# Kernel tuning notes

Measured on AMD Instinct MI355X. Metric: run time of the kernel, lower is better.

Reference implementation:

```python
import jax, jax.numpy as jnp
import numpy as np

N = 50000
E = 400000
C_IN = 32
H = 64
RATIO = 0.5
SEQ_LEN = 5


def setup_inputs() -> dict:
    key = jax.random.key(0)
    ks = jax.random.split(key, 12)
    x = jax.random.normal(ks[0], (N, C_IN), jnp.float32)
    row = jax.random.randint(ks[1], (E,), 0, N, jnp.int32)
    off = jax.random.randint(ks[2], (E,), 1, N, jnp.int32)
    col = ((row + off) % N).astype(jnp.int32)  # no self-loops
    edge_index = jnp.stack([row, col])
    mask = jax.random.uniform(ks[3], (N,)) < 0.5

    def g(k, shape, fan):
        return jax.random.normal(k, shape, jnp.float32) / np.float32(np.sqrt(fan))

    return {
        "x": x, "edge_index": edge_index, "mask": mask,
        "conv0_w": g(ks[4], (C_IN, H), C_IN), "conv0_b": jnp.zeros((H,), jnp.float32),
        "conv1_w": g(ks[5], (H, H), H), "conv1_b": jnp.zeros((H,), jnp.float32),
        "pool_w": g(ks[6], (H,), H),
        "up_w": g(ks[7], (H, H), H), "up_b": jnp.zeros((H,), jnp.float32),
        "lstm0_w_ih": g(ks[8], (4 * H, H), H), "lstm0_w_hh": g(ks[9], (4 * H, H), H),
        "lstm0_b_ih": jnp.zeros((4 * H,), jnp.float32), "lstm0_b_hh": jnp.zeros((4 * H,), jnp.float32),
        "fin_w_ih": g(ks[10], (4 * H, H), H), "fin_w_hh": g(ks[11], (4 * H, H), H),
        "fin_b_ih": jnp.zeros((4 * H,), jnp.float32), "fin_b_hh": jnp.zeros((4 * H,), jnp.float32),
    }


def _coalesce(row, col, w, n):
    # sum duplicate (row, col) entries; output sorted by (row, col)
    key = row.astype(np.int64) * n + col.astype(np.int64)
    uk, inv = np.unique(key, return_inverse=True)
    w2 = np.bincount(inv, weights=w.astype(np.float64), minlength=uk.shape[0]).astype(np.float32)
    return uk // n, uk % n, w2


def _augment_adj(row, col, w, n):
    # remove self loops, add self loops (weight 1), compute A @ A (sparse), remove self loops
    m = row != col
    row = np.concatenate([row[m].astype(np.int64), np.arange(n, dtype=np.int64)])
    col = np.concatenate([col[m].astype(np.int64), np.arange(n, dtype=np.int64)])
    w = np.concatenate([w[m].astype(np.float32), np.ones(n, np.float32)])
    row, col, w = _coalesce(row, col, w, n)  # CSR-ordered
    cnt = np.bincount(row, minlength=n)
    indptr = np.concatenate([[0], np.cumsum(cnt)])
    dk = cnt[col]                      # out-degree of middle node k for each edge (i,k)
    starts = indptr[col]
    total = int(dk.sum())
    seg = np.repeat(np.cumsum(dk) - dk, dk)
    gi = np.repeat(starts, dk) + (np.arange(total) - seg)
    oi = np.repeat(row, dk)
    oj = col[gi]
    ow = np.repeat(w, dk) * w[gi]
    r2, c2, w2 = _coalesce(oi, oj, ow, n)
    m2 = r2 != c2
    return r2[m2], c2[m2], w2[m2]


def _gcn(x, row, col, ew, n, W, b):
    # GCNConv(improved=True): self-loop weight 2.0, symmetric deg^-1/2 normalization,
    # aggregate messages at target (col)
    h = x @ W
    loop = jnp.arange(n, dtype=row.dtype)
    r = jnp.concatenate([row, loop])
    c = jnp.concatenate([col, loop])
    w = jnp.concatenate([ew, jnp.full((n,), 2.0, ew.dtype)])
    deg = jax.ops.segment_sum(w, c, num_segments=n)
    dinv = jnp.where(deg > 0, jax.lax.rsqrt(deg), 0.0)
    norm = dinv[r] * w * dinv[c]
    out = jax.ops.segment_sum(norm[:, None] * h[r], c, num_segments=n)
    return out + b


def _sequences(x, mi):
    # sliding window [idx-L+1, idx] per masked node, zero left-padded
    t = mi[:, None] + jnp.arange(SEQ_LEN)[None, :] - (SEQ_LEN - 1)  # [M, L]
    return jnp.where((t >= 0)[:, :, None], x[jnp.clip(t, 0)], 0.0)


def _lstm_last(seq, w_ih, w_hh, b_ih, b_hh):
    # torch LSTM gate order: i, f, g, o; zero init state; return last hidden
    h = jnp.zeros((seq.shape[0], w_hh.shape[1]), seq.dtype)
    c = jnp.zeros_like(h)
    def step(carry, xt):
        h, c = carry
        g = xt @ w_ih.T + h @ w_hh.T + b_ih + b_hh
        i, f, gg, o = jnp.split(g, 4, axis=-1)
        c = jax.nn.sigmoid(f) * c + jax.nn.sigmoid(i) * jnp.tanh(gg)
        h = jax.nn.sigmoid(o) * jnp.tanh(c)
        return (h, c), None
    (h, _), _ = jax.lax.scan(step, (h, c), jnp.swapaxes(seq, 0, 1))
    return h


def reference(x, edge_index, mask, conv0_w, conv0_b, conv1_w, conv1_b, pool_w,
              up_w, up_b, lstm0_w_ih, lstm0_w_hh, lstm0_b_ih, lstm0_b_hh,
              fin_w_ih, fin_w_hh, fin_b_ih, fin_b_hh):
    n = x.shape[0]
    row0, col0 = edge_index[0], edge_index[1]
    ew0 = jnp.ones((row0.shape[0],), x.dtype)

    # down conv 0
    x1 = jax.nn.relu(_gcn(x, row0, col0, ew0, n, conv0_w, conv0_b))

    # augment_adj: sparse (A+I)^2 without diagonal (structural, constant)
    r2, c2, w2 = _augment_adj(np.asarray(row0), np.asarray(col0),
                              np.ones(row0.shape[0], np.float32), n)

    # TopKPooling: score = tanh((x.w)/||w||), keep top ceil(ratio*n)
    score = jnp.tanh((x1 @ pool_w) / jnp.linalg.norm(pool_w))
    k = int(np.ceil(RATIO * n))
    perm = np.argsort(-np.asarray(score), kind="stable")[:k]
    remap = np.full(n, -1, np.int64)
    remap[perm] = np.arange(k)
    keep = (remap[r2] >= 0) & (remap[c2] >= 0)
    pr = jnp.asarray(remap[r2[keep]].astype(np.int32))
    pc = jnp.asarray(remap[c2[keep]].astype(np.int32))
    pw = jnp.asarray(w2[keep])
    permj = jnp.asarray(perm.astype(np.int32))
    xp = x1[permj] * score[permj][:, None]

    # down conv 1 on pooled graph
    x2 = jax.nn.relu(_gcn(xp, pr, pc, pw, k, conv1_w, conv1_b))

    # up path (depth=1): LSTM over skip features at masked nodes
    mi = jnp.asarray(np.where(np.asarray(mask))[0].astype(np.int32))
    h0 = _lstm_last(_sequences(x1, mi), lstm0_w_ih, lstm0_w_hh, lstm0_b_ih, lstm0_b_hh)
    res = x1.at[mi].set(h0)
    up = jnp.zeros_like(x1).at[permj].set(x2)
    xo = _gcn(res + up, row0, col0, ew0, n, up_w, up_b)  # last level: no activation

    # final LSTM on masked nodes
    hf = _lstm_last(_sequences(xo, mi), fin_w_ih, fin_w_hh, fin_b_ih, fin_b_hh)
    return xo.at[mi].set(hf)
```

## Files before the change

### kernel.cpp

```cpp
#include <hip/hip_runtime.h>
#include <math.h>

#define NN 50000
#define EE 400000
#define CINV 32
#define KKEEP 25000
#define SEQL 5
#define HASH_BITS 20
#define HASH_SIZE (1u<<HASH_BITS)
#define HASH_MASK (HASH_SIZE-1u)
#define HEMPTY 0xFFFFFFFFu
#define PSB 196

typedef float vf4 __attribute__((ext_vector_type(4)));

__device__ __forceinline__ float sigm(float x){ return __builtin_amdgcn_rcpf(1.f+__expf(-x)); }
__device__ __forceinline__ float ftanh(float x){ return 1.f - 2.f*__builtin_amdgcn_rcpf(1.f+__expf(2.f*x)); }

__global__ void k_init(uint2* __restrict__ hash, unsigned* __restrict__ hist,
                       int* __restrict__ degcnt, int* __restrict__ diagint,
                       int* __restrict__ fillc, int* __restrict__ minv,
                       unsigned* scal, unsigned long long* selp,
                       const float* __restrict__ w0, const float* __restrict__ b0i,
                       const float* __restrict__ b0h, const float* __restrict__ wf,
                       const float* __restrict__ bfi, const float* __restrict__ bfh,
                       float* __restrict__ WT0, float* __restrict__ WTf,
                       float* __restrict__ bs0, float* __restrict__ bsf){
  int i = blockIdx.x*256 + threadIdx.x;
  if (i < (int)HASH_SIZE) hash[i] = make_uint2(HEMPTY, 0u);
  if (i < 4*65536) hist[i] = 0u;
  if (i < NN){ degcnt[i]=0; diagint[i]=0; fillc[i]=0; minv[i]=-1; }
  if (i < 256*64){
    int g = i>>6, k = i&63;
    WT0[k*256+g] = w0[i];
    WTf[k*256+g] = wf[i];
  }
  if (i < 256){ bs0[i]=b0i[i]+b0h[i]; bsf[i]=bfi[i]+bfh[i]; }
  if (i == 0){ scal[0]=0u; scal[1]=0u; scal[3]=KKEEP; selp[0]=0ull; }
}

__global__ void k_phase2(const int* __restrict__ row, const int* __restrict__ col,
                         const int* __restrict__ mp, int* __restrict__ degcnt,
                         uint2* __restrict__ tab, unsigned* scal,
                         const float* __restrict__ X, const float* __restrict__ W,
                         float* __restrict__ Y){
  int idx = blockIdx.x*256 + threadIdx.x;
  if (idx < EE){
    int c = col[idx];
    atomicAdd(&degcnt[c], 1);
    unsigned key = (unsigned)row[idx]*50000u + (unsigned)c;
    unsigned h = (key*2654435761u) >> (32-HASH_BITS);
    for(;;){
      unsigned old = atomicCAS(&tab[h].x, HEMPTY, key);
      if (old==HEMPTY || old==key){ atomicAdd(&tab[h].y, 1u); break; }
      h = (h+1)&HASH_MASK;
    }
  }
  if (idx < NN/4){ if ((unsigned)mp[idx] > 1u) atomicOr(&scal[1], 1u); }
  if (idx < NN*16){
    int i = idx>>4, fq = idx&15;
    const vf4* X4 = (const vf4*)&X[i*CINV];
    const vf4* W4 = (const vf4*)W;
    vf4 acc = {0.f,0.f,0.f,0.f};
    #pragma unroll
    for (int kq=0;kq<CINV/4;kq++){
      vf4 xv = X4[kq];
      #pragma unroll
      for (int u=0;u<4;u++) acc += xv[u] * W4[(kq*4+u)*16+fq];
    }
    ((vf4*)Y)[i*16+fq] = acc;
  }
}

__global__ void k_psum1(const int* __restrict__ deg, int* __restrict__ part,
                        int* __restrict__ bsum, float* __restrict__ dinv){
  __shared__ int sc[256];
  int b = blockIdx.x, t = threadIdx.x, i = b*256+t;
  int v = (i<NN) ? deg[i] : 0;
  if (i < NN) dinv[i] = rsqrtf((float)v + 2.0f);
  sc[t] = v; __syncthreads();
  for (int o=1;o<256;o<<=1){
    int x = (t>=o) ? sc[t-o] : 0;
    __syncthreads();
    sc[t] += x;
    __syncthreads();
  }
  if (i < NN) part[i] = sc[t]-v;
  if (t == 255) bsum[b] = sc[255];
}
__global__ void k_psum3(const int* __restrict__ part, const int* __restrict__ bsum,
                        int* __restrict__ indptr){
  __shared__ int sc[256];
  int t = threadIdx.x;
  int v = (t<PSB) ? bsum[t] : 0;
  sc[t] = v; __syncthreads();
  for (int o=1;o<256;o<<=1){
    int x = (t>=o) ? sc[t-o] : 0;
    __syncthreads();
    sc[t] += x;
    __syncthreads();
  }
  int bb = blockIdx.x;
  int ex = sc[bb] - ((bb<PSB) ? bsum[bb] : 0);
  int i = bb*256 + t;
  if (i < NN) indptr[i] = part[i] + ex;
  if (i == 0) indptr[NN] = EE;
}

__global__ void k_phase4(const int* __restrict__ row, const int* __restrict__ col,
                         const int* __restrict__ indptr, int* __restrict__ fillc,
                         int* __restrict__ csr_r, const uint2* __restrict__ tab,
                         int* __restrict__ diagint, const void* __restrict__ mp,
                         unsigned* scal, int* __restrict__ mlist, int* __restrict__ minv){
  int idx = blockIdx.x*256 + threadIdx.x;
  if (idx < EE){
    int r = row[idx], c = col[idx];
    int pos = indptr[c] + atomicAdd(&fillc[c], 1);
    csr_r[pos] = r;
    unsigned rkey = (unsigned)c*50000u + (unsigned)r;
    unsigned h = (rkey*2654435761u) >> (32-HASH_BITS);
    for(;;){
      unsigned kk = tab[h].x;
      if (kk==rkey){ atomicAdd(&diagint[r], (int)tab[h].y); break; }
      if (kk==HEMPTY) break;
      h = (h+1)&HASH_MASK;
    }
  } else {
    int i = idx - EE;
    if (i < NN){
      int mv = scal[1] ? (int)((const unsigned char*)mp)[i] : ((const int*)mp)[i];
      if (mv){ int p = (int)atomicAdd(&scal[0], 1u); mlist[p] = i; minv[i] = p; }
    }
  }
}

__global__ void k_mm64v(const float* __restrict__ X, const float* __restrict__ W, float* __restrict__ Y){
  int idx = blockIdx.x*256 + threadIdx.x;
  if (idx >= NN*16) return;
  int i = idx>>4, fq = idx&15;
  const vf4* X4 = (const vf4*)&X[i*64];
  const vf4* W4 = (const vf4*)W;
  vf4 acc = {0.f,0.f,0.f,0.f};
  #pragma unroll
  for (int kq=0;kq<16;kq++){
    vf4 xv = X4[kq];
    #pragma unroll
    for (int u=0;u<4;u++) acc += xv[u] * W4[(kq*4+u)*16+fq];
  }
  ((vf4*)Y)[i*16+fq] = acc;
}

__global__ void g_gcn0(const int* __restrict__ indptr, const int* __restrict__ csr_r,
                       const float* __restrict__ dinv, const float* __restrict__ H,
                       const float* __restrict__ b, const float* __restrict__ pw,
                       float* __restrict__ out, unsigned long long* __restrict__ keys,
                       float* __restrict__ score, unsigned* __restrict__ hist){
  int node = blockIdx.x*4 + (threadIdx.x>>6), lane = threadIdx.x&63;
  if (node >= NN) return;
  int s = __builtin_amdgcn_readfirstlane(indptr[node]);
  int e = __builtin_amdgcn_readfirstlane(indptr[node+1]);
  int deg = e - s;
  float a0=0.f,a1=0.f,a2=0.f,a3=0.f;
  for (int base=0; base<deg; base+=64){
    int take = min(64, deg-base);
    bool act = lane < take;
    int ii = act ? csr_r[s+base+lane] : 0;
    float dv = act ? dinv[ii] : 0.f;
    int j=0;
    for (; j+4<=take; j+=4){
      int r0=__shfl(ii,j,64), r1=__shfl(ii,j+1,64), r2=__shfl(ii,j+2,64), r3=__shfl(ii,j+3,64);
      float d0=__shfl(dv,j,64), d1=__shfl(dv,j+1,64), d2=__shfl(dv,j+2,64), d3=__shfl(dv,j+3,64);
      a0 += d0*H[(size_t)r0*64+lane];
      a1 += d1*H[(size_t)r1*64+lane];
      a2 += d2*H[(size_t)r2*64+lane];
      a3 += d3*H[(size_t)r3*64+lane];
    }
    for (; j<take; j++){
      int r0=__shfl(ii,j,64); float d0=__shfl(dv,j,64);
      a0 += d0*H[(size_t)r0*64+lane];
    }
  }
  float acc = (a0+a1)+(a2+a3);
  float di = dinv[node];
  float v = di*acc + 2.f*di*di*H[(size_t)node*64+lane] + b[lane];
  float x1v = fmaxf(v, 0.f);
  out[(size_t)node*64+lane] = x1v;
  float pv = pw[lane];
  float nq = pv*pv;
  float dq = x1v*pv;
  for (int o=32;o;o>>=1){ nq += __shfl_down(nq, o, 64); dq += __shfl_down(dq, o, 64); }
  if (lane==0){
    float sv = tanhf(dq / sqrtf(nq));
    sv = sv + 0.0f;
    score[node] = sv;
    unsigned u = __float_as_uint(sv);
    unsigned asc = (u>>31) ? ~u : (u | 0x80000000u);
    unsigned desc = ~asc;
    keys[node] = (((unsigned long long)desc)<<32) | (unsigned)node;
    atomicAdd(&hist[desc>>16], 1u);
  }
}
__global__ void g_t2(const int* __restrict__ indptr, const int* __restrict__ csr_r,
                     const float* __restrict__ dinv1, const float* __restrict__ hp,
                     float* __restrict__ t2){
  int node = blockIdx.x*4 + (threadIdx.x>>6), lane = threadIdx.x&63;
  if (node >= NN) return;
  int s = __builtin_amdgcn_readfirstlane(indptr[node]);
  int e = __builtin_amdgcn_readfirstlane(indptr[node+1]);
  int deg = e - s;
  float a0 = dinv1[node]*hp[(size_t)node*64+lane];
  float a1 = 0.f;
  for (int base=0; base<deg; base+=64){
    int take = min(64, deg-base);
    bool act = lane < take;
    int ii = act ? csr_r[s+base+lane] : 0;
    float dv = act ? dinv1[ii] : 0.f;
    int j=0;
    for (; j+2<=take; j+=2){
      float d0=__shfl(dv,j,64), d1=__shfl(dv,j+1,64);
      int r0=__shfl(ii,j,64), r1=__shfl(ii,j+1,64);
      if (d0!=0.f) a0 += d0*hp[(size_t)r0*64+lane];
      if (d1!=0.f) a1 += d1*hp[(size_t)r1*64+lane];
    }
    for (; j<take; j++){
      float d0=__shfl(dv,j,64); int r0=__shfl(ii,j,64);
      if (d0!=0.f) a0 += d0*hp[(size_t)r0*64+lane];
    }
  }
  t2[(size_t)node*64+lane] = a0+a1;
}
__global__ void g_agg2y(const int* __restrict__ indptr, const int* __restrict__ csr_r,
                        const float* __restrict__ t2, const float* __restrict__ hp,
                        const float* __restrict__ dinv1, const int* __restrict__ diagint,
                        const int* __restrict__ kp, const float* __restrict__ b1,
                        const float* __restrict__ C, const float* __restrict__ Hbuf,
                        const int* __restrict__ minv, float* __restrict__ D){
  int node = blockIdx.x*4 + (threadIdx.x>>6), lane = threadIdx.x&63;
  if (node >= NN) return;
  int mv = minv[node];
  float base = (mv >= 0) ? Hbuf[(size_t)mv*64+lane] : C[(size_t)node*64+lane];
  float add = 0.f;
  if (kp[node]){
    int s = __builtin_amdgcn_readfirstlane(indptr[node]);
    int e = __builtin_amdgcn_readfirstlane(indptr[node+1]);
    int deg = e - s;
    float a0 = t2[(size_t)node*64+lane];
    float a1=0.f,a2=0.f,a3=0.f;
    for (int bs2=0; bs2<deg; bs2+=64){
      int take = min(64, deg-bs2);
      bool act = lane < take;
      int ii = act ? csr_r[s+bs2+lane] : 0;
      int j=0;
      for (; j+4<=take; j+=4){
        int r0=__shfl(ii,j,64), r1=__shfl(ii,j+1,64), r2=__shfl(ii,j+2,64), r3=__shfl(ii,j+3,64);
        a0 += t2[(size_t)r0*64+lane];
        a1 += t2[(size_t)r1*64+lane];
        a2 += t2[(size_t)r2*64+lane];
        a3 += t2[(size_t)r3*64+lane];
      }
      for (; j<take; j++){
        int r0=__shfl(ii,j,64);
        a0 += t2[(size_t)r0*64+lane];
      }
    }
    float acc = (a0+a1)+(a2+a3);
    float di = dinv1[node], hv = hp[(size_t)node*64+lane];
    float diag = (float)(diagint[node] + 1);
    float v = di*(acc - diag*di*hv) + 2.f*di*di*hv + b1[lane];
    add = fmaxf(v, 0.f);
  }
  D[(size_t)node*64+lane] = base + add;
}
__global__ void g_up(const int* __restrict__ indptr, const int* __restrict__ csr_r,
                     const float* __restrict__ dinv, const float* __restrict__ H,
                     const float* __restrict__ b, float* __restrict__ xo, float* __restrict__ out){
  int node = blockIdx.x*4 + (threadIdx.x>>6), lane = threadIdx.x&63;
  if (node >= NN) return;
  int s = __builtin_amdgcn_readfirstlane(indptr[node]);
  int e = __builtin_amdgcn_readfirstlane(indptr[node+1]);
  int deg = e - s;
  float a0=0.f,a1=0.f,a2=0.f,a3=0.f;
  for (int base=0; base<deg; base+=64){
    int take = min(64, deg-base);
    bool act = lane < take;
    int ii = act ? csr_r[s+base+lane] : 0;
    float dv = act ? dinv[ii] : 0.f;
    int j=0;
    for (; j+4<=take; j+=4){
      int r0=__shfl(ii,j,64), r1=__shfl(ii,j+1,64), r2=__shfl(ii,j+2,64), r3=__shfl(ii,j+3,64);
      float d0=__shfl(dv,j,64), d1=__shfl(dv,j+1,64), d2=__shfl(dv,j+2,64), d3=__shfl(dv,j+3,64);
      a0 += d0*H[(size_t)r0*64+lane];
      a1 += d1*H[(size_t)r1*64+lane];
      a2 += d2*H[(size_t)r2*64+lane];
      a3 += d3*H[(size_t)r3*64+lane];
    }
    for (; j<take; j++){
      int r0=__shfl(ii,j,64); float d0=__shfl(dv,j,64);
      a0 += d0*H[(size_t)r0*64+lane];
    }
  }
  float acc = (a0+a1)+(a2+a3);
  float di = dinv[node];
  float v = di*acc + 2.f*di*di*H[(size_t)node*64+lane] + b[lane];
  xo[(size_t)node*64+lane] = v; out[(size_t)node*64+lane] = v;
}

__global__ void k_hist(const unsigned long long* __restrict__ keys, unsigned* __restrict__ hist,
                       const unsigned long long* __restrict__ selp, int round){
  int i = blockIdx.x*256 + threadIdx.x;
  if (i >= NN) return;
  unsigned long long key = keys[i];
  int shift = 48 - 16*round;
  if ((key>>(shift+16)) == selp[0])
    atomicAdd(&hist[(unsigned)((key>>shift)&0xFFFFull)], 1u);
}
__global__ void k_pick(const unsigned* __restrict__ hist, unsigned long long* selp, unsigned* scal){
  __shared__ unsigned csum[256];
  __shared__ unsigned bins[256];
  __shared__ int schunk;
  int t = threadIdx.x;
  const uint4* h4 = (const uint4*)(hist + t*256);
  unsigned s = 0;
  #pragma unroll 8
  for (int j=0;j<64;j++){ uint4 v = h4[j]; s += v.x+v.y+v.z+v.w; }
  csum[t] = s;
  __syncthreads();
  if (t==0){
    unsigned rem = scal[3];
    int chunk = 255;
    for (int c2=0;c2<256;c2++){ unsigned cc=csum[c2]; if (rem>cc) rem-=cc; else { chunk=c2; break; } }
    schunk = chunk; scal[3] = rem;
  }
  __syncthreads();
  bins[t] = hist[schunk*256 + t];
  __syncthreads();
  if (t==0){
    unsigned rem = scal[3];
    int bin = schunk*256 + 255;
    for (int b=0;b<256;b++){ unsigned hv=bins[b]; if (rem>hv) rem-=hv; else { bin = schunk*256 + b; break; } }
    selp[0] = (selp[0]<<16) | (unsigned long long)(unsigned)bin;
    scal[3] = rem;
  }
}
__global__ void k_tsg(const int* __restrict__ indptr, const int* __restrict__ csr_r,
                      const unsigned long long* __restrict__ keys,
                      const unsigned long long* __restrict__ selp,
                      int* __restrict__ kp, int* __restrict__ ts){
  int i = blockIdx.x*256 + threadIdx.x;
  if (i >= NN) return;
  unsigned long long sp = selp[0];
  int s = indptr[i], e = indptr[i+1];
  int self = (keys[i] <= sp) ? 1 : 0;
  kp[i] = self;
  int acc = self;
  for (int j=s;j<e;j++) acc += (keys[csr_r[j]] <= sp) ? 1 : 0;
  ts[i] = acc;
}
__global__ void k_csgmm(const int* __restrict__ indptr, const int* __restrict__ csr_r,
                        const int* __restrict__ ts, const int* __restrict__ diagint,
                        const int* __restrict__ kp, float* __restrict__ dinv1,
                        const float* __restrict__ X, const float* __restrict__ W,
                        const float* __restrict__ sc, float* __restrict__ Y){
  int idx = blockIdx.x*256 + threadIdx.x;
  if (idx < NN*16){
    int i = idx>>4, fq = idx&15;
    if (!kp[i]) return;
    const vf4* X4 = (const vf4*)&X[i*64];
    const vf4* W4 = (const vf4*)W;
    vf4 acc = {0.f,0.f,0.f,0.f};
    #pragma unroll
    for (int kq=0;kq<16;kq++){
      vf4 xv = X4[kq];
      #pragma unroll
      for (int u=0;u<4;u++) acc += xv[u] * W4[(kq*4+u)*16+fq];
    }
    acc *= sc[i];
    ((vf4*)Y)[i*16+fq] = acc;
  } else {
    int i = idx - NN*16;
    if (i >= NN) return;
    int s = indptr[i], e = indptr[i+1];
    int acc = ts[i];
    for (int j=s;j<e;j++) acc += ts[csr_r[j]];
    dinv1[i] = kp[i] ? rsqrtf((float)(acc - diagint[i] - 1) + 2.0f) : 0.f;
  }
}

__global__ __launch_bounds__(256) void k_xw(const float* __restrict__ src,
        const float* __restrict__ WT, const float* __restrict__ bsum,
        float* __restrict__ XW){
  __shared__ vf4 Wl[4096];
  int t = threadIdx.x;
  const vf4* Wg = (const vf4*)WT;
  for (int u=t; u<4096; u+=256) Wl[u] = Wg[u];
  int fq = t & 63, wv = t >> 6;
  vf4 bias = ((const vf4*)bsum)[fq];
  __syncthreads();
  for (int g = blockIdx.x*4 + wv; g < NN/4; g += gridDim.x*4){
    int n0 = g*4;
    const vf4* X4 = (const vf4*)&src[(size_t)n0*64];
    vf4 a0=bias, a1=bias, a2=bias, a3=bias;
    #pragma unroll 4
    for (int kq=0;kq<16;kq++){
      vf4 x0 = X4[kq], x1 = X4[16+kq], x2 = X4[32+kq], x3 = X4[48+kq];
      vf4 w0 = Wl[(kq*4+0)*64+fq];
      vf4 w1 = Wl[(kq*4+1)*64+fq];
      vf4 w2 = Wl[(kq*4+2)*64+fq];
      vf4 w3 = Wl[(kq*4+3)*64+fq];
      a0 += x0.x*w0 + x0.y*w1 + x0.z*w2 + x0.w*w3;
      a1 += x1.x*w0 + x1.y*w1 + x1.z*w2 + x1.w*w3;
      a2 += x2.x*w0 + x2.y*w1 + x2.z*w2 + x2.w*w3;
      a3 += x3.x*w0 + x3.y*w1 + x3.z*w2 + x3.w*w3;
    }
    vf4* Y = (vf4*)XW;
    Y[(size_t)n0*64 + fq]       = a0;
    Y[(size_t)n0*64 + 64 + fq]  = a1;
    Y[(size_t)n0*64 + 128 + fq] = a2;
    Y[(size_t)n0*64 + 192 + fq] = a3;
  }
}

__global__ __launch_bounds__(256) void k_rec(const float* __restrict__ XW,
        const float* __restrict__ whh, const float* __restrict__ bsum,
        const int* __restrict__ mlist, const unsigned* __restrict__ scal,
        float* __restrict__ dst, int scatter){
  int M = (int)scal[0];
  if (M < 0 || M > NN) M = 0;
  int w = threadIdx.x>>6, lane = threadIdx.x&63;
  int r = w*64 + lane;
  const vf4* g4 = (const vf4*)&whh[(size_t)r*64];
  vf4 wh[16];
  #pragma unroll
  for (int j=0;j<16;j++) wh[j] = g4[j];
  __shared__ float sh[4][64];
  __shared__ float gates[4][4][64];
  int ntask = (M+3)>>2;
  for (int task = blockIdx.x; task < ntask; task += gridDim.x){
    int m = task*4 + w;
    bool valid = (m < M);
    int node = mlist[valid ? m : (M-1)];
    node = min(max(node, 0), NN-1);
    float c, h;
    float x0,x1,x2,x3;
    {
      int rowi = node - (SEQL-1);
      if (rowi >= 0){
        const float* p = &XW[(size_t)rowi*256];
        x0=p[lane]; x1=p[64+lane]; x2=p[128+lane]; x3=p[192+lane];
      } else {
        x0=bsum[lane]; x1=bsum[64+lane]; x2=bsum[128+lane]; x3=bsum[192+lane];
      }
      c = sigm(x0)*ftanh(x2);
      h = sigm(x3)*ftanh(c);
      sh[w][lane] = h;
    }
    __syncthreads();
    for (int t=1;t<SEQL;t++){
      int rowi = node - (SEQL-1) + t;
      if (rowi >= 0){
        const float* p = &XW[(size_t)rowi*256];
        x0=p[lane]; x1=p[64+lane]; x2=p[128+lane]; x3=p[192+lane];
      } else {
        x0=bsum[lane]; x1=bsum[64+lane]; x2=bsum[128+lane]; x3=bsum[192+lane];
      }
      vf4 a0={0,0,0,0}, a1={0,0,0,0}, a2={0,0,0,0}, a3={0,0,0,0};
      #pragma unroll
      for (int j=0;j<16;j++){
        vf4 wj = wh[j];
        a0 += (*(const vf4*)&sh[0][j*4]) * wj;
        a1 += (*(const vf4*)&sh[1][j*4]) * wj;
        a2 += (*(const vf4*)&sh[2][j*4]) * wj;
        a3 += (*(const vf4*)&sh[3][j*4]) * wj;
      }
      gates[0][w][lane] = a0.x+a0.y+a0.z+a0.w;
      gates[1][w][lane] = a1.x+a1.y+a1.z+a1.w;
      gates[2][w][lane] = a2.x+a2.y+a2.z+a2.w;
      gates[3][w][lane] = a3.x+a3.y+a3.z+a3.w;
      __syncthreads();
      float gi = gates[w][0][lane] + x0;
      float gf = gates[w][1][lane] + x1;
      float gg = gates[w][2][lane] + x2;
      float go = gates[w][3][lane] + x3;
      c = sigm(gf)*c + sigm(gi)*ftanh(gg);
      h = sigm(go)*ftanh(c);
      sh[w][lane] = h;
      __syncthreads();
    }
    if (valid){
      size_t o = scatter ? ((size_t)node*64 + lane) : ((size_t)m*64 + lane);
      dst[o] = h;
    }
  }
}

extern "C" void kernel_launch(void* const* d_in, const int* in_sizes, int n_in,
                              void* d_out, int out_size, void* d_ws, size_t ws_size,
                              hipStream_t stream) {
  const float* x   = (const float*)d_in[0];
  const int*   ei  = (const int*)d_in[1];
  const int*   row = ei;
  const int*   col = ei + EE;
  const void*  mp  = d_in[2];
  const float* W0  = (const float*)d_in[3];
  const float* b0  = (const float*)d_in[4];
  const float* W1  = (const float*)d_in[5];
  const float* b1  = (const float*)d_in[6];
  const float* pw  = (const float*)d_in[7];
  const float* Wu  = (const float*)d_in[8];
  const float* bu  = (const float*)d_in[9];
  const float* l0wih=(const float*)d_in[10];
  const float* l0whh=(const float*)d_in[11];
  const float* l0bih=(const float*)d_in[12];
  const float* l0bhh=(const float*)d_in[13];
  const float* lfwih=(const float*)d_in[14];
  const float* lfwhh=(const float*)d_in[15];
  const float* lfbih=(const float*)d_in[16];
  const float* lfbhh=(const float*)d_in[17];

  char* wp = (char*)d_ws;
  auto alloc = [&](size_t bytes)->char*{ char* p = wp; wp += ((bytes+255)/256)*256; return p; };
  float* A     = (float*)alloc((size_t)NN*64*4);
  float* B     = (float*)alloc((size_t)NN*64*4);
  float* C     = (float*)alloc((size_t)NN*64*4);
  float* D     = (float*)alloc((size_t)NN*64*4);
  float* Ebuf  = (float*)alloc((size_t)NN*64*4);
  float* Hbuf  = (float*)alloc((size_t)NN*64*4);
  float* XW    = (float*)alloc((size_t)NN*256*4);
  float* WT0   = (float*)alloc((size_t)256*64*4);
  float* WTf   = (float*)alloc((size_t)256*64*4);
  float* bs0   = (float*)alloc((size_t)256*4);
  float* bsf   = (float*)alloc((size_t)256*4);
  float* score = (float*)alloc((size_t)NN*4);
  float* dinv0 = (float*)alloc((size_t)NN*4);
  float* dinv1 = (float*)alloc((size_t)NN*4);
  unsigned long long* keys = (unsigned long long*)alloc((size_t)NN*8);
  int* degcnt  = (int*)alloc((size_t)NN*4);
  int* diagint = (int*)alloc((size_t)NN*4);
  int* ts      = (int*)alloc((size_t)NN*4);
  int* kp      = (int*)alloc((size_t)NN*4);
  int* mlist   = (int*)alloc((size_t)NN*4);
  int* minv    = (int*)alloc((size_t)NN*4);
  int* indptr  = (int*)alloc((size_t)(NN+1)*4);
  int* part    = (int*)alloc((size_t)NN*4);
  int* fillc   = (int*)alloc((size_t)NN*4);
  int* bsum    = (int*)alloc((size_t)256*4);
  int* csr_r   = (int*)alloc((size_t)EE*4);
  uint2* hash  = (uint2*)alloc((size_t)HASH_SIZE*8);
  unsigned* hist=(unsigned*)alloc((size_t)4*65536*4);
  unsigned* scal=(unsigned*)alloc(256);
  unsigned long long* selp = (unsigned long long*)(scal + 4);

  #define GRID1(n) dim3(((n)+255)/256), dim3(256), 0, stream
  #define GRIDW dim3((NN+3)/4), dim3(256), 0, stream

  k_init<<<GRID1(HASH_SIZE)>>>(hash, hist, degcnt, diagint, fillc, minv,
                               scal, selp, l0wih, l0bih, l0bhh, lfwih, lfbih, lfbhh,
                               WT0, WTf, bs0, bsf);
  k_phase2<<<GRID1(NN*16)>>>(row, col, (const int*)mp, degcnt, hash, scal, x, W0, A);
  k_psum1<<<dim3(PSB),dim3(256),0,stream>>>(degcnt, part, bsum, dinv0);
  k_psum3<<<dim3(PSB),dim3(256),0,stream>>>(part, bsum, indptr);
  k_phase4<<<GRID1(EE+NN)>>>(row, col, indptr, fillc, csr_r, hash, diagint, mp, scal, mlist, minv);

  g_gcn0<<<GRIDW>>>(indptr, csr_r, dinv0, A, b0, pw, C, keys, score, hist);

  k_pick<<<dim3(1),dim3(256),0,stream>>>(hist, selp, scal);
  for (int r2=1;r2<4;r2++){
    k_hist<<<GRID1(NN)>>>(keys, hist + r2*65536, selp, r2);
    k_pick<<<dim3(1),dim3(256),0,stream>>>(hist + r2*65536, selp, scal);
  }
  k_tsg<<<GRID1(NN)>>>(indptr, csr_r, keys, selp, kp, ts);
  k_csgmm<<<GRID1(NN*16+NN)>>>(indptr, csr_r, ts, diagint, kp, dinv1, C, W1, score, Ebuf);
  g_t2<<<GRIDW>>>(indptr, csr_r, dinv1, Ebuf, A);

  k_xw<<<dim3(512),dim3(256),0,stream>>>(C, WT0, bs0, XW);
  k_rec<<<dim3(1024),dim3(256),0,stream>>>(XW, l0whh, bs0, mlist, scal, Hbuf, 0);

  g_agg2y<<<GRIDW>>>(indptr, csr_r, A, Ebuf, dinv1, diagint, kp, b1, C, Hbuf, minv, D);

  k_mm64v<<<GRID1(NN*16)>>>(D, Wu, Ebuf);
  g_up<<<GRIDW>>>(indptr, csr_r, dinv0, Ebuf, bu, B, (float*)d_out);

  k_xw<<<dim3(512),dim3(256),0,stream>>>(B, WTf, bsf, XW);
  k_rec<<<dim3(1024),dim3(256),0,stream>>>(XW, lfwhh, bsf, mlist, scal, (float*)d_out, 1);
  #undef GRIDW
  #undef GRID1
}
```

Measured before the change: 651.4 us.

## Restructure LSTM recurrence so each wave owns two sequences with full W_hh in registers

The LSTM recurrence kernel is reorganised so each wavefront processes two masked-node sequences independently. Each lane keeps all four gate weights for its hidden unit in registers (W_hh is pre-transposed in the init kernel into a lane-friendly layout). This removes the block-wide __syncthreads and the shared gate-exchange buffer, leaving only per-wave LDS for h. The cost is 256 weight VGPRs per lane, forcing one block per SM and a smaller grid, which lowers occupancy and risks register spills.

```diff
diff --git a/kernel.cpp b/kernel.cpp
--- a/kernel.cpp
+++ b/kernel.cpp
@@ -24,16 +24,21 @@
                        const float* __restrict__ w0, const float* __restrict__ b0i,
                        const float* __restrict__ b0h, const float* __restrict__ wf,
                        const float* __restrict__ bfi, const float* __restrict__ bfh,
+                       const float* __restrict__ whh0, const float* __restrict__ whhf,
                        float* __restrict__ WT0, float* __restrict__ WTf,
+                       float* __restrict__ WHT0, float* __restrict__ WHTf,
                        float* __restrict__ bs0, float* __restrict__ bsf){
   int i = blockIdx.x*256 + threadIdx.x;
   if (i < (int)HASH_SIZE) hash[i] = make_uint2(HEMPTY, 0u);
   if (i < 4*65536) hist[i] = 0u;
   if (i < NN){ degcnt[i]=0; diagint[i]=0; fillc[i]=0; minv[i]=-1; }
   if (i < 256*64){
-    int g = i>>6, k = i&63;
-    WT0[k*256+g] = w0[i];
-    WTf[k*256+g] = wf[i];
+    int r = i>>6, k = i&63;
+    WT0[k*256+r] = w0[i];
+    WTf[k*256+r] = wf[i];
+    int dst = (((k>>2)*4 + (r>>6))*64 + (r&63))*4 + (k&3);
+    WHT0[dst] = whh0[i];
+    WHTf[dst] = whhf[i];
   }
   if (i < 256){ bs0[i]=b0i[i]+b0h[i]; bsf[i]=bfi[i]+bfh[i]; }
   if (i == 0){ scal[0]=0u; scal[1]=0u; scal[3]=KKEEP; selp[0]=0ull; }
@@ -420,76 +425,72 @@
   }
 }
 
-__global__ __launch_bounds__(256) void k_rec(const float* __restrict__ XW,
-        const float* __restrict__ whh, const float* __restrict__ bsum,
+__global__ __launch_bounds__(256, 1) void k_rec(const float* __restrict__ XW,
+        const float* __restrict__ WHT, const float* __restrict__ bsum,
         const int* __restrict__ mlist, const unsigned* __restrict__ scal,
         float* __restrict__ dst, int scatter){
   int M = (int)scal[0];
   if (M < 0 || M > NN) M = 0;
   int w = threadIdx.x>>6, lane = threadIdx.x&63;
-  int r = w*64 + lane;
-  const vf4* g4 = (const vf4*)&whh[(size_t)r*64];
-  vf4 wh[16];
+  vf4 wr[64];
+  const vf4* WT4 = (const vf4*)WHT;
   #pragma unroll
-  for (int j=0;j<16;j++) wh[j] = g4[j];
-  __shared__ float sh[4][64];
-  __shared__ float gates[4][4][64];
-  int ntask = (M+3)>>2;
+  for (int j=0;j<64;j++) wr[j] = WT4[j*64 + lane];
+  __shared__ __align__(16) float sh[4][2][64];
+  float* shA = &sh[w][0][0];
+  float* shB = &sh[w][1][0];
+  float b0v = bsum[lane], b1v = bsum[64+lane], b2v = bsum[128+lane], b3v = bsum[192+lane];
+  int ntask = (M+7)>>3;
   for (int task = blockIdx.x; task < ntask; task += gridDim.x){
-    int m = task*4 + w;
-    bool valid = (m < M);
-    int node = mlist[valid ? m : (M-1)];
-    node = min(max(node, 0), NN-1);
-    float c, h;
-    float x0,x1,x2,x3;
+    int mA = task*8 + w*2, mB = mA + 1;
+    bool vA = (mA < M), vB = (mB < M);
+    int nodeA = mlist[vA ? mA : 0]; nodeA = min(max(nodeA,0),NN-1);
+    int nodeB = mlist[vB ? mB : 0]; nodeB = min(max(nodeB,0),NN-1);
+    float cA,hA,cB,hB;
+    float xA0,xA1,xA2,xA3, xB0,xB1,xB2,xB3;
     {
-      int rowi = node - (SEQL-1);
-      if (rowi >= 0){
-        const float* p = &XW[(size_t)rowi*256];
-        x0=p[lane]; x1=p[64+lane]; x2=p[128+lane]; x3=p[192+lane];
-      } else {
-        x0=bsum[lane]; x1=bsum[64+lane]; x2=bsum[128+lane]; x3=bsum[192+lane];
+      int rA = nodeA - (SEQL-1), rB = nodeB - (SEQL-1);
+      if (rA >= 0){ const float* p=&XW[(size_t)rA*256]; xA0=p[lane];xA1=p[64+lane];xA2=p[128+lane];xA3=p[192+lane]; }
+      else { xA0=b0v;xA1=b1v;xA2=b2v;xA3=b3v; }
+      if (rB >= 0){ const float* p=&XW[(size_t)rB*256]; xB0=p[lane];xB1=p[64+lane];xB2=p[128+lane];xB3=p[192+lane]; }
+      else { xB0=b0v;xB1=b1v;xB2=b2v;xB3=b3v; }
+      cA = sigm(xA0)*ftanh(xA2); hA = sigm(xA3)*ftanh(cA);
+      cB = sigm(xB0)*ftanh(xB2); hB = sigm(xB3)*ftanh(cB);
+      shA[lane] = hA; shB[lane] = hB;
+    }
+    for (int t=1;t<SEQL;t++){
+      int rA = nodeA - (SEQL-1) + t, rB = nodeB - (SEQL-1) + t;
+      if (rA >= 0){ const float* p=&XW[(size_t)rA*256]; xA0=p[lane];xA1=p[64+lane];xA2=p[128+lane];xA3=p[192+lane]; }
+      else { xA0=b0v;xA1=b1v;xA2=b2v;xA3=b3v; }
+      if (rB >= 0){ const float* p=&XW[(size_t)rB*256]; xB0=p[lane];xB1=p[64+lane];xB2=p[128+lane];xB3=p[192+lane]; }
+      else { xB0=b0v;xB1=b1v;xB2=b2v;xB3=b3v; }
+      asm volatile("s_waitcnt lgkmcnt(0)" ::: "memory");
+      __builtin_amdgcn_sched_barrier(0);
+      vf4 aA0={0,0,0,0},aA1={0,0,0,0},aA2={0,0,0,0},aA3={0,0,0,0};
+      vf4 aB0={0,0,0,0},aB1={0,0,0,0},aB2={0,0,0,0},aB3={0,0,0,0};
+      #pragma unroll
+      for (int kq=0;kq<16;kq++){
+        vf4 ha = *(const vf4*)&shA[kq*4];
+        vf4 hb = *(const vf4*)&shB[kq*4];
+        aA0 += ha*wr[kq*4+0]; aA1 += ha*wr[kq*4+1]; aA2 += ha*wr[kq*4+2]; aA3 += ha*wr[kq*4+3];
+        aB0 += hb*wr[kq*4+0]; aB1 += hb*wr[kq*4+1]; aB2 += hb*wr[kq*4+2]; aB3 += hb*wr[kq*4+3];
       }
-      c = sigm(x0)*ftanh(x2);
-      h = sigm(x3)*ftanh(c);
-      sh[w][lane] = h;
-    }
-    __syncthreads();
-    for (int t=1;t<SEQL;t++){
-      int rowi = node - (SEQL-1) + t;
-      if (rowi >= 0){
-        const float* p = &XW[(size_t)rowi*256];
-        x0=p[lane]; x1=p[64+lane]; x2=p[128+lane]; x3=p[192+lane];
-      } else {
-        x0=bsum[lane]; x1=bsum[64+lane]; x2=bsum[128+lane]; x3=bsum[192+lane];
-      }
-      vf4 a0={0,0,0,0}, a1={0,0,0,0}, a2={0,0,0,0}, a3={0,0,0,0};
-      #pragma unroll
-      for (int j=0;j<16;j++){
-        vf4 wj = wh[j];
-        a0 += (*(const vf4*)&sh[0][j*4]) * wj;
-        a1 += (*(const vf4*)&sh[1][j*4]) * wj;
-        a2 += (*(const vf4*)&sh[2][j*4]) * wj;
-        a3 += (*(const vf4*)&sh[3][j*4]) * wj;
-      }
-      gates[0][w][lane] = a0.x+a0.y+a0.z+a0.w;
-      gates[1][w][lane] = a1.x+a1.y+a1.z+a1.w;
-      gates[2][w][lane] = a2.x+a2.y+a2.z+a2.w;
-      gates[3][w][lane] = a3.x+a3.y+a3.z+a3.w;
-      __syncthreads();
-      float gi = gates[w][0][lane] + x0;
-      float gf = gates[w][1][lane] + x1;
-      float gg = gates[w][2][lane] + x2;
-      float go = gates[w][3][lane] + x3;
-      c = sigm(gf)*c + sigm(gi)*ftanh(gg);
-      h = sigm(go)*ftanh(c);
-      sh[w][lane] = h;
-      __syncthreads();
-    }
-    if (valid){
-      size_t o = scatter ? ((size_t)node*64 + lane) : ((size_t)m*64 + lane);
-      dst[o] = h;
-    }
+      float gAi = aA0.x+aA0.y+aA0.z+aA0.w + xA0;
+      float gAf = aA1.x+aA1.y+aA1.z+aA1.w + xA1;
+      float gAg = aA2.x+aA2.y+aA2.z+aA2.w + xA2;
+      float gAo = aA3.x+aA3.y+aA3.z+aA3.w + xA3;
+      cA = sigm(gAf)*cA + sigm(gAi)*ftanh(gAg);
+      hA = sigm(gAo)*ftanh(cA);
+      float gBi = aB0.x+aB0.y+aB0.z+aB0.w + xB0;
+      float gBf = aB1.x+aB1.y+aB1.z+aB1.w + xB1;
+      float gBg = aB2.x+aB2.y+aB2.z+aB2.w + xB2;
+      float gBo = aB3.x+aB3.y+aB3.z+aB3.w + xB3;
+      cB = sigm(gBf)*cB + sigm(gBi)*ftanh(gBg);
+      hB = sigm(gBo)*ftanh(cB);
+      if (t < SEQL-1){ shA[lane] = hA; shB[lane] = hB; }
+    }
+    if (vA){ size_t o = scatter ? ((size_t)nodeA*64 + lane) : ((size_t)mA*64 + lane); dst[o] = hA; }
+    if (vB){ size_t o = scatter ? ((size_t)nodeB*64 + lane) : ((size_t)mB*64 + lane); dst[o] = hB; }
   }
 }
 
@@ -528,6 +529,8 @@
   float* XW    = (float*)alloc((size_t)NN*256*4);
   float* WT0   = (float*)alloc((size_t)256*64*4);
   float* WTf   = (float*)alloc((size_t)256*64*4);
+  float* WHT0  = (float*)alloc((size_t)256*64*4);
+  float* WHTf  = (float*)alloc((size_t)256*64*4);
   float* bs0   = (float*)alloc((size_t)256*4);
   float* bsf   = (float*)alloc((size_t)256*4);
   float* score = (float*)alloc((size_t)NN*4);
@@ -555,7 +558,7 @@
 
   k_init<<<GRID1(HASH_SIZE)>>>(hash, hist, degcnt, diagint, fillc, minv,
                                scal, selp, l0wih, l0bih, l0bhh, lfwih, lfbih, lfbhh,
-                               WT0, WTf, bs0, bsf);
+                               l0whh, lfwhh, WT0, WTf, WHT0, WHTf, bs0, bsf);
   k_phase2<<<GRID1(NN*16)>>>(row, col, (const int*)mp, degcnt, hash, scal, x, W0, A);
   k_psum1<<<dim3(PSB),dim3(256),0,stream>>>(degcnt, part, bsum, dinv0);
   k_psum3<<<dim3(PSB),dim3(256),0,stream>>>(part, bsum, indptr);
@@ -573,7 +576,7 @@
   g_t2<<<GRIDW>>>(indptr, csr_r, dinv1, Ebuf, A);
 
   k_xw<<<dim3(512),dim3(256),0,stream>>>(C, WT0, bs0, XW);
-  k_rec<<<dim3(1024),dim3(256),0,stream>>>(XW, l0whh, bs0, mlist, scal, Hbuf, 0);
+  k_rec<<<dim3(256),dim3(256),0,stream>>>(XW, WHT0, bs0, mlist, scal, Hbuf, 0);
 
   g_agg2y<<<GRIDW>>>(indptr, csr_r, A, Ebuf, dinv1, diagint, kp, b1, C, Hbuf, minv, D);
 
@@ -581,7 +584,7 @@
   g_up<<<GRIDW>>>(indptr, csr_r, dinv0, Ebuf, bu, B, (float*)d_out);
 
   k_xw<<<dim3(512),dim3(256),0,stream>>>(B, WTf, bsf, XW);
-  k_rec<<<dim3(1024),dim3(256),0,stream>>>(XW, lfwhh, bsf, mlist, scal, (float*)d_out, 1);
+  k_rec<<<dim3(256),dim3(256),0,stream>>>(XW, WHTf, bsf, mlist, scal, (float*)d_out, 1);
   #undef GRIDW
   #undef GRID1
 }
```

Result: slower. 1.250 ms (+92.0%).

## Interleave LSTM input-projection gates and prefetch timesteps in one-task-per-block recurrence

Applied to the files above, without the earlier changes.

The input-projection weights and biases are permuted so each node's four gate values for a hidden unit sit together and load as one float4. The recurrence kernel now runs one task per block on a grid of 12500, with blocks past the masked count returning early, and it prefetches later timestep rows before they are needed. The intent is fewer scattered scalar loads, latency hidden behind the recurrent matvec, and no grid-stride loop. In exchange, each block reloads its whh registers and many blocks are launched.

```diff
diff --git a/kernel.cpp b/kernel.cpp
--- a/kernel.cpp
+++ b/kernel.cpp
@@ -31,11 +31,15 @@
   if (i < 4*65536) hist[i] = 0u;
   if (i < NN){ degcnt[i]=0; diagint[i]=0; fillc[i]=0; minv[i]=-1; }
   if (i < 256*64){
-    int g = i>>6, k = i&63;
-    WT0[k*256+g] = w0[i];
-    WTf[k*256+g] = wf[i];
-  }
-  if (i < 256){ bs0[i]=b0i[i]+b0h[i]; bsf[i]=bfi[i]+bfh[i]; }
+    int r = i>>6, k = i&63;
+    int dst = k*256 + (r&63)*4 + (r>>6);
+    WT0[dst] = w0[i];
+    WTf[dst] = wf[i];
+  }
+  if (i < 256){
+    int dst = (i&63)*4 + (i>>6);
+    bs0[dst]=b0i[i]+b0h[i]; bsf[dst]=bfi[i]+bfh[i];
+  }
   if (i == 0){ scal[0]=0u; scal[1]=0u; scal[3]=KKEEP; selp[0]=0ull; }
 }
 
@@ -426,6 +430,8 @@
         float* __restrict__ dst, int scatter){
   int M = (int)scal[0];
   if (M < 0 || M > NN) M = 0;
+  int task = blockIdx.x;
+  if (task*4 >= M) return;
   int w = threadIdx.x>>6, lane = threadIdx.x&63;
   int r = w*64 + lane;
   const vf4* g4 = (const vf4*)&whh[(size_t)r*64];
@@ -434,62 +440,57 @@
   for (int j=0;j<16;j++) wh[j] = g4[j];
   __shared__ float sh[4][64];
   __shared__ float gates[4][4][64];
-  int ntask = (M+3)>>2;
-  for (int task = blockIdx.x; task < ntask; task += gridDim.x){
-    int m = task*4 + w;
-    bool valid = (m < M);
-    int node = mlist[valid ? m : (M-1)];
-    node = min(max(node, 0), NN-1);
-    float c, h;
-    float x0,x1,x2,x3;
-    {
-      int rowi = node - (SEQL-1);
-      if (rowi >= 0){
-        const float* p = &XW[(size_t)rowi*256];
-        x0=p[lane]; x1=p[64+lane]; x2=p[128+lane]; x3=p[192+lane];
-      } else {
-        x0=bsum[lane]; x1=bsum[64+lane]; x2=bsum[128+lane]; x3=bsum[192+lane];
-      }
-      c = sigm(x0)*ftanh(x2);
-      h = sigm(x3)*ftanh(c);
-      sh[w][lane] = h;
-    }
+  int m = task*4 + w;
+  bool valid = (m < M);
+  int node = mlist[valid ? m : (M-1)];
+  node = min(max(node, 0), NN-1);
+  const vf4* XW4 = (const vf4*)XW;
+  vf4 bp = ((const vf4*)bsum)[lane];
+  vf4 xs0, xs1, xs2, xs3, xs4;
+  {
+    int r0 = node - 4, r1 = node - 3;
+    xs0 = (r0 >= 0) ? XW4[(size_t)r0*64 + lane] : bp;
+    xs1 = (r1 >= 0) ? XW4[(size_t)r1*64 + lane] : bp;
+  }
+  float c, h;
+  {
+    c = sigm(xs0.x)*ftanh(xs0.z);
+    h = sigm(xs0.w)*ftanh(c);
+    sh[w][lane] = h;
+  }
+  __syncthreads();
+  #pragma unroll
+  for (int t=1;t<SEQL;t++){
+    if (t==1){ int ri = node-2; xs2 = (ri>=0) ? XW4[(size_t)ri*64+lane] : bp; }
+    if (t==2){ int ri = node-1; xs3 = (ri>=0) ? XW4[(size_t)ri*64+lane] : bp; }
+    if (t==3){ xs4 = XW4[(size_t)node*64 + lane]; }
+    vf4 a0={0,0,0,0}, a1={0,0,0,0}, a2={0,0,0,0}, a3={0,0,0,0};
+    #pragma unroll
+    for (int j=0;j<16;j++){
+      vf4 wj = wh[j];
+      a0 += (*(const vf4*)&sh[0][j*4]) * wj;
+      a1 += (*(const vf4*)&sh[1][j*4]) * wj;
+      a2 += (*(const vf4*)&sh[2][j*4]) * wj;
+      a3 += (*(const vf4*)&sh[3][j*4]) * wj;
+    }
+    gates[0][w][lane] = a0.x+a0.y+a0.z+a0.w;
+    gates[1][w][lane] = a1.x+a1.y+a1.z+a1.w;
+    gates[2][w][lane] = a2.x+a2.y+a2.z+a2.w;
+    gates[3][w][lane] = a3.x+a3.y+a3.z+a3.w;
     __syncthreads();
-    for (int t=1;t<SEQL;t++){
-      int rowi = node - (SEQL-1) + t;
-      if (rowi >= 0){
-        const float* p = &XW[(size_t)rowi*256];
-        x0=p[lane]; x1=p[64+lane]; x2=p[128+lane]; x3=p[192+lane];
-      } else {
-        x0=bsum[lane]; x1=bsum[64+lane]; x2=bsum[128+lane]; x3=bsum[192+lane];
-      }
-      vf4 a0={0,0,0,0}, a1={0,0,0,0}, a2={0,0,0,0}, a3={0,0,0,0};
-      #pragma unroll
-      for (int j=0;j<16;j++){
-        vf4 wj = wh[j];
-        a0 += (*(const vf4*)&sh[0][j*4]) * wj;
-        a1 += (*(const vf4*)&sh[1][j*4]) * wj;
-        a2 += (*(const vf4*)&sh[2][j*4]) * wj;
-        a3 += (*(const vf4*)&sh[3][j*4]) * wj;
-      }
-      gates[0][w][lane] = a0.x+a0.y+a0.z+a0.w;
-      gates[1][w][lane] = a1.x+a1.y+a1.z+a1.w;
-      gates[2][w][lane] = a2.x+a2.y+a2.z+a2.w;
-      gates[3][w][lane] = a3.x+a3.y+a3.z+a3.w;
-      __syncthreads();
-      float gi = gates[w][0][lane] + x0;
-      float gf = gates[w][1][lane] + x1;
-      float gg = gates[w][2][lane] + x2;
-      float go = gates[w][3][lane] + x3;
-      c = sigm(gf)*c + sigm(gi)*ftanh(gg);
-      h = sigm(go)*ftanh(c);
-      sh[w][lane] = h;
-      __syncthreads();
-    }
-    if (valid){
-      size_t o = scatter ? ((size_t)node*64 + lane) : ((size_t)m*64 + lane);
-      dst[o] = h;
-    }
+    vf4 xv = (t==1) ? xs1 : (t==2) ? xs2 : (t==3) ? xs3 : xs4;
+    float gi = gates[w][0][lane] + xv.x;
+    float gf = gates[w][1][lane] + xv.y;
+    float gg = gates[w][2][lane] + xv.z;
+    float go = gates[w][3][lane] + xv.w;
+    c = sigm(gf)*c + sigm(gi)*ftanh(gg);
+    h = sigm(go)*ftanh(c);
+    sh[w][lane] = h;
+    __syncthreads();
+  }
+  if (valid){
+    size_t o = scatter ? ((size_t)node*64 + lane) : ((size_t)m*64 + lane);
+    dst[o] = h;
   }
 }
 
@@ -573,7 +574,7 @@
   g_t2<<<GRIDW>>>(indptr, csr_r, dinv1, Ebuf, A);
 
   k_xw<<<dim3(512),dim3(256),0,stream>>>(C, WT0, bs0, XW);
-  k_rec<<<dim3(1024),dim3(256),0,stream>>>(XW, l0whh, bs0, mlist, scal, Hbuf, 0);
+  k_rec<<<dim3(12500),dim3(256),0,stream>>>(XW, l0whh, bs0, mlist, scal, Hbuf, 0);
 
   g_agg2y<<<GRIDW>>>(indptr, csr_r, A, Ebuf, dinv1, diagint, kp, b1, C, Hbuf, minv, D);
 
@@ -581,7 +582,7 @@
   g_up<<<GRIDW>>>(indptr, csr_r, dinv0, Ebuf, bu, B, (float*)d_out);
 
   k_xw<<<dim3(512),dim3(256),0,stream>>>(B, WTf, bsf, XW);
-  k_rec<<<dim3(1024),dim3(256),0,stream>>>(XW, lfwhh, bsf, mlist, scal, (float*)d_out, 1);
+  k_rec<<<dim3(12500),dim3(256),0,stream>>>(XW, lfwhh, bsf, mlist, scal, (float*)d_out, 1);
   #undef GRIDW
   #undef GRID1
 }
```

Result: no change. 648.5 us (-0.4%).
